# Performance work log

Measured on AMD Instinct MI355X. Metric: run time of the kernel, lower is better.

The kernel has to match this reference:

```python
import jax, jax.numpy as jnp
import numpy as np

NUM_DIRECTIONS = 100  # matches init_kwargs
N_POINTS = 200000


def setup_inputs() -> dict:
    key = jax.random.key(0)
    k1, k2 = jax.random.split(key)
    X = jax.random.normal(k1, (N_POINTS, 2), dtype=jnp.float32)
    Y = jax.random.normal(k2, (N_POINTS, 2), dtype=jnp.float32)
    return {"X": X, "Y": Y}


def _lines():
    # thetas = linspace(-pi/2, pi/2, K+1)[:-1]; lines[i] = (cos t_i, sin t_i)
    thetas = jnp.linspace(-np.pi / 2, np.pi / 2, NUM_DIRECTIONS + 1)[:-1]
    L = jnp.stack([jnp.cos(thetas), jnp.sin(thetas)], axis=1).astype(jnp.float32)  # [K, 2]
    return L


def reference(X, Y):
    # X, Y: [N, 2], [M, 2] persistence diagrams (birth, death)
    L = _lines()                                   # [K, 2]
    inv_norm = 1.0 / jnp.sum(L * L, axis=1)        # [K] (== 1 analytically, kept for fidelity)
    diag = jnp.array([0.5, 0.5], dtype=jnp.float32)

    # diagonal projections of each diagram: sum(point) * [0.5, 0.5]
    X_diag = jnp.sum(X, axis=1, keepdims=True) * diag  # [N, 2]
    Y_diag = jnp.sum(Y, axis=1, keepdims=True) * diag  # [M, 2]

    # batched line projections: replaces per-point dot-product loops
    proj_X = (X @ L.T) * inv_norm                  # [N, K]
    proj_Y = (Y @ L.T) * inv_norm                  # [M, K]
    proj_Xd = (X_diag @ L.T) * inv_norm            # [N, K]
    proj_Yd = (Y_diag @ L.T) * inv_norm            # [M, K]

    # 1D EMD per direction: sort both multisets, sum |diff|
    A = jnp.sort(jnp.concatenate([proj_X, proj_Yd], axis=0), axis=0)  # [N+M, K]
    B = jnp.sort(jnp.concatenate([proj_Y, proj_Xd], axis=0), axis=0)  # [N+M, K]

    total_cost = jnp.sum(jnp.abs(A - B)) / NUM_DIRECTIONS
    return total_cost
```

## Files before the change

kernel.cpp:

```cpp
#include <hip/hip_runtime.h>

#define KDIR 100
#define TILE 4096
#define NPASS 3
#define MBLK 256
#define MOUT 4096
#define MPT2 (MOUT / MBLK)

__device__ __forceinline__ unsigned encodeF(float f) {
  unsigned u = __float_as_uint(f);
  return u ^ ((u >> 31) ? 0xFFFFFFFFu : 0x80000000u);
}
__device__ __forceinline__ float decodeU(unsigned u) {
  return __uint_as_float(u ^ ((u >> 31) ? 0x80000000u : 0xFFFFFFFFu));
}

__global__ void k_table(float* tbl, double* part, int nSlots) {
  int k = threadIdx.x;
  const double PI = 3.14159265358979323846;
  if (k < KDIR) {
    double th = -PI * 0.5 + (double)k * (PI / (double)KDIR);
    float c = (float)cos(th), s = (float)sin(th);
    float invn = 1.0f / (c * c + s * s);
    tbl[k] = c; tbl[128 + k] = s; tbl[256 + k] = (c + s) * invn; tbl[384 + k] = invn;
  }
  if (k == 100) { tbl[100] = 0.5f; tbl[228] = 0.5f; tbl[484] = 1.0f; }
  for (int i = k; i < nSlots; i += 256) part[i] = 0.0;
}

__global__ __launch_bounds__(256) void k_build(const float* __restrict__ P, int n, int kIdx,
                                               const float* __restrict__ tbl,
                                               unsigned* __restrict__ dst,
                                               unsigned* __restrict__ counts, int T, int seg0) {
  __shared__ unsigned h[256];
  int tid = threadIdx.x;
  h[tid] = 0;
  __syncthreads();
  int dir = blockIdx.y;
  int k = kIdx + dir;
  float ck = tbl[k], sk = tbl[128 + k], inv = tbl[384 + k];
  int tile = blockIdx.x;
  int start = tile * TILE;
  int nItems = min(TILE, n - start);
  unsigned* d0 = dst + (size_t)dir * n + start;
  const float* p0 = P + 2 * (size_t)start;
  if (nItems == TILE) {
    const float4* p4 = (const float4*)p0;
    uint2* o2 = (uint2*)d0;
#pragma unroll
    for (int i = 0; i < 8; ++i) {
      float4 v = p4[i * 256 + tid];
      unsigned ua = encodeF((v.x * ck + v.y * sk) * inv);
      unsigned ub = encodeF((v.z * ck + v.w * sk) * inv);
      o2[i * 256 + tid] = make_uint2(ua, ub);
      atomicAdd(&h[(ua >> 8) & 255u], 1u);
      atomicAdd(&h[(ub >> 8) & 255u], 1u);
    }
  } else {
    for (int j = tid; j < nItems; j += 256) {
      float x = p0[2 * j], y = p0[2 * j + 1];
      unsigned u = encodeF((x * ck + y * sk) * inv);
      d0[j] = u;
      atomicAdd(&h[(u >> 8) & 255u], 1u);
    }
  }
  __syncthreads();
  counts[((size_t)(seg0 + dir) * 256 + tid) * T + tile] = h[tid];
}

__global__ __launch_bounds__(256) void k_hist8(const unsigned* __restrict__ keys,
                                               int L, int T, int shift,
                                               unsigned* __restrict__ counts) {
  __shared__ unsigned h[4][256];
  int tid = threadIdx.x;
  int w = tid >> 6;
  for (int i = tid; i < 4 * 256; i += 256) ((unsigned*)h)[i] = 0;
  __syncthreads();
  int seg = blockIdx.y, tile = blockIdx.x;
  const unsigned* base = keys + (size_t)seg * L + (size_t)tile * TILE;
  int nItems = min(TILE, L - tile * TILE);
  if (nItems == TILE) {
    const uint4* b4 = (const uint4*)base;
#pragma unroll
    for (int i = 0; i < 4; ++i) {
      uint4 v = b4[i * 256 + tid];
      atomicAdd(&h[w][(v.x >> shift) & 255u], 1u);
      atomicAdd(&h[w][(v.y >> shift) & 255u], 1u);
      atomicAdd(&h[w][(v.z >> shift) & 255u], 1u);
      atomicAdd(&h[w][(v.w >> shift) & 255u], 1u);
    }
  } else {
    for (int i = tid; i < nItems; i += 256)
      atomicAdd(&h[w][(base[i] >> shift) & 255u], 1u);
  }
  __syncthreads();
  counts[((size_t)seg * 256 + tid) * T + tile] =
      h[0][tid] + h[1][tid] + h[2][tid] + h[3][tid];
}

__global__ __launch_bounds__(256) void k_scanSeg(unsigned* __restrict__ counts, int T) {
  __shared__ unsigned tot[256];
  unsigned* c = counts + (size_t)blockIdx.x * 256 * T;
  int tid = threadIdx.x;
  int base = tid * T;
  unsigned sum = 0;
  for (int i = 0; i < T; ++i) sum += c[base + i];
  tot[tid] = sum;
  __syncthreads();
  for (int ofs = 1; ofs < 256; ofs <<= 1) {
    unsigned t = (tid >= ofs) ? tot[tid - ofs] : 0u;
    __syncthreads();
    tot[tid] += t;
    __syncthreads();
  }
  unsigned run = tot[tid] - sum;
  for (int i = 0; i < T; ++i) {
    unsigned v = c[base + i];
    c[base + i] = run;
    run += v;
  }
}

__global__ __launch_bounds__(256) void k_scatter8(const unsigned* __restrict__ src,
                                                  unsigned* __restrict__ dst,
                                                  int L, int T, int shift,
                                                  const unsigned* __restrict__ counts) {
  __shared__ unsigned runG[4][4][256];
  __shared__ unsigned diffD[256];
  __shared__ unsigned wsum[4];
  int tid = threadIdx.x;
  int lane = tid & 63, w = tid >> 6;
  int seg = blockIdx.y, tile = blockIdx.x;
  const unsigned* sbase = src + (size_t)seg * L + (size_t)tile * TILE;
  int nItems = min(TILE, L - tile * TILE);
  for (int i = tid; i < 4 * 4 * 256; i += 256) ((unsigned*)runG)[i] = 0;
  __syncthreads();
  unsigned kk[16];
  unsigned rr[16];
  unsigned long long laneLT = (1ull << lane) - 1ull;
  int jbase = w * (TILE / 4);
#pragma unroll
  for (int i = 0; i < 16; ++i) {
    int j = jbase + i * 64 + lane;
    kk[i] = (j < nItems) ? sbase[j] : 0xFFFFFFFFu;
  }
#pragma unroll
  for (int s = 0; s < 4; ++s) {
    unsigned long long mask[4];
    unsigned prev[4];
#pragma unroll
    for (int g = 0; g < 4; ++g) {
      int i = g * 4 + s;
      int j = jbase + i * 64 + lane;
      bool valid = j < nItems;
      unsigned long long act = __ballot(valid);
      unsigned d = (kk[i] >> shift) & 255u;
      unsigned long long m = act;
#pragma unroll
      for (int b = 0; b < 8; ++b) {
        unsigned long long bal = __ballot((d >> b) & 1);
        m &= ((d >> b) & 1) ? bal : ~bal;
      }
      mask[g] = m;
      prev[g] = runG[w][g][d];
    }
#pragma unroll
    for (int g = 0; g < 4; ++g) {
      int i = g * 4 + s;
      int j = jbase + i * 64 + lane;
      if (j < nItems) {
        unsigned d = (kk[i] >> shift) & 255u;
        unsigned r = (unsigned)__popcll(mask[g] & laneLT);
        rr[i] = prev[g] + r;
        if (r == 0) runG[w][g][d] = prev[g] + (unsigned)__popcll(mask[g]);
      }
    }
  }
  __syncthreads();
  {
    unsigned v[16];
#pragma unroll
    for (int w2 = 0; w2 < 4; ++w2)
#pragma unroll
      for (int g2 = 0; g2 < 4; ++g2) v[w2 * 4 + g2] = runG[w2][g2][tid];
    unsigned tot = 0;
#pragma unroll
    for (int i = 0; i < 16; ++i) {
      unsigned t = v[i];
      v[i] = tot;
      tot += t;
    }
    unsigned x = tot;
#pragma unroll
    for (int ofs = 1; ofs < 64; ofs <<= 1) {
      unsigned t = __shfl_up(x, ofs, 64);
      if (lane >= ofs) x += t;
    }
    if (lane == 63) wsum[w] = x;
    __syncthreads();
    unsigned basew = 0;
#pragma unroll
    for (int w2 = 0; w2 < 4; ++w2) basew += (w2 < w) ? wsum[w2] : 0u;
    unsigned localStart = basew + x - tot;
    diffD[tid] = counts[((size_t)seg * 256 + tid) * T + tile] - localStart;
#pragma unroll
    for (int w2 = 0; w2 < 4; ++w2)
#pragma unroll
      for (int g2 = 0; g2 < 4; ++g2)
        runG[w2][g2][tid] = v[w2 * 4 + g2] + localStart;
  }
  __syncthreads();
  unsigned lp[16];
#pragma unroll
  for (int i = 0; i < 16; ++i) {
    unsigned d = (kk[i] >> shift) & 255u;
    lp[i] = runG[w][i >> 2][d] + rr[i];
  }
  __syncthreads();
  unsigned* kbuf = &runG[0][0][0];
#pragma unroll
  for (int i = 0; i < 16; ++i) {
    int j = jbase + i * 64 + lane;
    if (j < nItems) kbuf[lp[i]] = kk[i];
  }
  __syncthreads();
  unsigned* dbase = dst + (size_t)seg * L;
#pragma unroll
  for (int i = 0; i < 16; ++i) {
    int pos = i * 256 + tid;
    if (pos < nItems) {
      unsigned k = kbuf[pos];
      unsigned d = (k >> shift) & 255u;
      dbase[diffD[d] + (unsigned)pos] = k;
    }
  }
}

__device__ __forceinline__ float scaledAt(const unsigned* __restrict__ s, int len, int j,
                                          float c, int rev) {
  return c * decodeU(s[rev ? (len - 1 - j) : j]);
}

__device__ int mergeSplit(const unsigned* __restrict__ U, int n,
                          const unsigned* __restrict__ sV, int m,
                          float c, int rev, int o) {
  int lo = o - m; if (lo < 0) lo = 0;
  int hi = o < n ? o : n;
  while (lo < hi) {
    int mid = (lo + hi + 1) >> 1;
    if (decodeU(U[mid - 1]) <= scaledAt(sV, m, o - mid, c, rev)) lo = mid;
    else hi = mid - 1;
  }
  return lo;
}

__global__ void k_splits(const unsigned* __restrict__ pX, const unsigned* __restrict__ pY,
                         const unsigned* __restrict__ sx, const unsigned* __restrict__ sy,
                         int N, int M, int k0, int mB,
                         const float* __restrict__ tbl, int* __restrict__ splits) {
  int b = blockIdx.x * blockDim.x + threadIdx.x;
  if (b >= mB) return;
  int kl = blockIdx.y;
  int kc = gridDim.y;
  float c = tbl[256 + k0 + kl];
  int rev = c < 0.0f ? 1 : 0;
  int Stot = N + M;
  int o = b * MOUT; if (o > Stot) o = Stot;
  const unsigned* U1 = pX + (size_t)kl * N;
  const unsigned* U2 = pY + (size_t)kl * M;
  splits[(size_t)kl * mB + b] = mergeSplit(U1, N, sy, M, c, rev, o);
  splits[((size_t)kc + kl) * mB + b] = mergeSplit(U2, M, sx, N, c, rev, o);
}

__device__ __forceinline__ int ldsSplit(const float* __restrict__ sArr, int aCnt, int bCnt,
                                        int o) {
  int lo = o - bCnt; if (lo < 0) lo = 0;
  int hi = o < aCnt ? o : aCnt;
  while (lo < hi) {
    int mid = (lo + hi + 1) >> 1;
    if (sArr[mid - 1] <= sArr[aCnt + o - mid]) lo = mid;
    else hi = mid - 1;
  }
  return lo;
}

__device__ __forceinline__ void merge8(const float* __restrict__ sArr, int aCnt, int bCnt,
                                       int la, int lb, float* m) {
  const float FMAX = 3.402823466e38f;
  float a[8], b[8];
#pragma unroll
  for (int j = 0; j < 8; ++j) {
    a[j] = (la + j < aCnt) ? sArr[la + j] : FMAX;
    b[j] = (lb + j < bCnt) ? sArr[aCnt + lb + j] : FMAX;
  }
#pragma unroll
  for (int j = 0; j < 8; ++j) m[j] = fminf(a[j], b[7 - j]);
#pragma unroll
  for (int d = 4; d > 0; d >>= 1) {
#pragma unroll
    for (int i = 0; i < 8; ++i) {
      if ((i & d) == 0 && (i | d) < 8) {
        float lo = fminf(m[i], m[i | d]);
        float hi = fmaxf(m[i], m[i | d]);
        m[i] = lo; m[i | d] = hi;
      }
    }
  }
}

__global__ __launch_bounds__(MBLK) void k_merge(const unsigned* __restrict__ pX,
                                                const unsigned* __restrict__ pY,
                                                const unsigned* __restrict__ sx,
                                                const unsigned* __restrict__ sy,
                                                int N, int M, int k0,
                                                const float* __restrict__ tbl,
                                                const int* __restrict__ splits, int mB,
                                                double* __restrict__ part) {
  __shared__ float sA[MOUT];
  __shared__ float sB[MOUT];
  __shared__ float red[MBLK];
  int kl = blockIdx.y;
  int kc = gridDim.y;
  float c = tbl[256 + k0 + kl];
  int rev = c < 0.0f ? 1 : 0;
  int Stot = N + M;
  int o0 = blockIdx.x * MOUT;
  int outCnt = min(MOUT, Stot - o0);
  const unsigned* U1 = pX + (size_t)kl * N;
  const unsigned* U2 = pY + (size_t)kl * M;
  int tid = threadIdx.x;
  int aLo = splits[(size_t)kl * mB + blockIdx.x];
  int aHi = splits[(size_t)kl * mB + blockIdx.x + 1];
  int a2Lo = splits[((size_t)kc + kl) * mB + blockIdx.x];
  int a2Hi = splits[((size_t)kc + kl) * mB + blockIdx.x + 1];
  int aCnt = aHi - aLo;
  int bLo = o0 - aLo, bCnt = outCnt - aCnt;
  int a2Cnt = a2Hi - a2Lo;
  int b2Lo = o0 - a2Lo, b2Cnt = outCnt - a2Cnt;
  for (int i = tid; i < aCnt; i += MBLK) sA[i] = decodeU(U1[aLo + i]);
  for (int i = tid; i < bCnt; i += MBLK) {
    int j = bLo + i;
    sA[aCnt + i] = c * decodeU(sy[rev ? (M - 1 - j) : j]);
  }
  for (int i = tid; i < a2Cnt; i += MBLK) sB[i] = decodeU(U2[a2Lo + i]);
  for (int i = tid; i < b2Cnt; i += MBLK) {
    int j = b2Lo + i;
    sB[a2Cnt + i] = c * decodeU(sx[rev ? (N - 1 - j) : j]);
  }
  __syncthreads();
  float acc = 0.0f;
#pragma unroll
  for (int half = 0; half < 2; ++half) {
    int lo0 = tid * MPT2 + half * 8;
    if (lo0 < outCnt) {
      int cnt = min(8, outCnt - lo0);
      int la = ldsSplit(sA, aCnt, bCnt, lo0);
      int lb = lo0 - la;
      int la2 = ldsSplit(sB, a2Cnt, b2Cnt, lo0);
      int lb2 = lo0 - la2;
      float mA[8], mB2[8];
      merge8(sA, aCnt, bCnt, la, lb, mA);
      merge8(sB, a2Cnt, b2Cnt, la2, lb2, mB2);
#pragma unroll
      for (int j = 0; j < 8; ++j)
        if (j < cnt) acc += fabsf(mA[j] - mB2[j]);
    }
  }
  red[tid] = acc;
  __syncthreads();
  for (int ofs = MBLK / 2; ofs > 0; ofs >>= 1) {
    if (tid < ofs) red[tid] += red[tid + ofs];
    __syncthreads();
  }
  if (tid == 0) {
    size_t slot = (size_t)(k0 + kl) * gridDim.x + blockIdx.x;
    part[slot] += (double)red[0];
  }
}

__global__ __launch_bounds__(256) void k_final(const double* __restrict__ part, int nSlots,
                                               float* __restrict__ out) {
  __shared__ double red[256];
  int tid = threadIdx.x;
  double s = 0.0;
  for (int i = tid; i < nSlots; i += 256) s += part[i];
  red[tid] = s;
  __syncthreads();
  for (int ofs = 128; ofs > 0; ofs >>= 1) {
    if (tid < ofs) red[tid] += red[tid + ofs];
    __syncthreads();
  }
  if (tid == 0) out[0] = (float)(red[0] / (double)KDIR);
}

extern "C" void kernel_launch(void* const* d_in, const int* in_sizes, int n_in,
                              void* d_out, int out_size, void* d_ws, size_t ws_size,
                              hipStream_t stream) {
  const float* X = (const float*)d_in[0];
  const float* Y = (const float*)d_in[1];
  int N = in_sizes[0] / 2;
  int M = in_sizes[1] / 2;

  char* ws = (char*)d_ws;
  size_t off = 0;
  auto alloc = [&](size_t b) -> void* {
    void* p = ws + off;
    off += (b + 255) & ~(size_t)255;
    return p;
  };
  float* tbl = (float*)alloc(512 * sizeof(float));
  unsigned* sPing = (unsigned*)alloc((size_t)(N + M) * 4);
  unsigned* sPong = (unsigned*)alloc((size_t)(N + M) * 4);

  int Tn = (N + TILE - 1) / TILE;
  int Tm = (M + TILE - 1) / TILE;
  int Tmax = Tn > Tm ? Tn : Tm;
  int mx = N > M ? N : M;
  int mBlocksAll = (N + M + MOUT - 1) / MOUT;
  int mB = mBlocksAll + 1;
  int nSlots = KDIR * mBlocksAll;
  int* splits = (int*)alloc((size_t)2 * KDIR * mB * 4);
  double* part = (double*)alloc((size_t)nSlots * 8);

  size_t perDir = (size_t)(N + M) * 8 + (size_t)2 * 256 * Tmax * 4;
  size_t reserve = (size_t)2 * mx * 8 + (size_t)2 * 256 * Tmax * 4;
  size_t remain = ws_size > off ? ws_size - off : 0;
  remain = remain > reserve ? remain - reserve : 0;
  int Kc = (int)(remain / perDir);
  if (Kc > KDIR) Kc = KDIR;
  if (Kc < 1) Kc = 1;
  int maxSegs = 2 * Kc + 2;
  unsigned* counts8 = (unsigned*)alloc((size_t)maxSegs * 256 * Tmax * 4);
  unsigned* cPing = (unsigned*)alloc(((size_t)Kc * (N + M) + 2 * (size_t)mx) * 4);
  unsigned* cPong = (unsigned*)alloc(((size_t)Kc * (N + M) + 2 * (size_t)mx) * 4);

  k_table<<<1, 256, 0, stream>>>(tbl, part, nSlots);

  auto sortJob = [&](unsigned* ping, unsigned* pong, int segs, int L) {
    int T = (L + TILE - 1) / TILE;
    unsigned* s = pong;
    unsigned* d = ping;
    for (int p = 0; p < NPASS; ++p) {
      int shift = 8 * (p + 1);
      if (p > 0)
        k_hist8<<<dim3(T, segs), 256, 0, stream>>>(s, L, T, shift, counts8);
      k_scanSeg<<<segs, 256, 0, stream>>>(counts8, T);
      k_scatter8<<<dim3(T, segs), 256, 0, stream>>>(s, d, L, T, shift, counts8);
      unsigned* t = s; s = d; d = t;
    }
  };

  bool fused = (N == M) && (Kc == KDIR);

  if (fused) {
    unsigned* dXin = cPong + (size_t)2 * KDIR * N;
    unsigned* dYin = dXin + N;
    k_build<<<dim3(Tn, KDIR), 256, 0, stream>>>(X, N, 0, tbl, cPong, counts8, Tn, 0);
    k_build<<<dim3(Tn, KDIR), 256, 0, stream>>>(Y, N, 0, tbl, cPong + (size_t)KDIR * N,
                                                counts8, Tn, KDIR);
    k_build<<<dim3(Tn, 1), 256, 0, stream>>>(X, N, 100, tbl, dXin, counts8, Tn, 2 * KDIR);
    k_build<<<dim3(Tn, 1), 256, 0, stream>>>(Y, N, 100, tbl, dYin, counts8, Tn, 2 * KDIR + 1);
    sortJob(cPing, cPong, 2 * KDIR + 2, N);
    unsigned* pX = cPing;
    unsigned* pY = cPing + (size_t)KDIR * N;
    unsigned* dX = cPing + (size_t)2 * KDIR * N;
    unsigned* dY = dX + N;
    k_splits<<<dim3((mB + 255) / 256, KDIR), 256, 0, stream>>>(pX, pY, dX, dY, N, M, 0, mB,
                                                               tbl, splits);
    k_merge<<<dim3(mBlocksAll, KDIR), MBLK, 0, stream>>>(pX, pY, dX, dY, N, M, 0, tbl,
                                                         splits, mB, part);
  } else {
    if (N == M) {
      k_build<<<dim3(Tn, 1), 256, 0, stream>>>(X, N, 100, tbl, sPong, counts8, Tn, 0);
      k_build<<<dim3(Tn, 1), 256, 0, stream>>>(Y, N, 100, tbl, sPong + N, counts8, Tn, 1);
      sortJob(sPing, sPong, 2, N);
    } else {
      k_build<<<dim3(Tn, 1), 256, 0, stream>>>(X, N, 100, tbl, sPong, counts8, Tn, 0);
      sortJob(sPing, sPong, 1, N);
      k_build<<<dim3(Tm, 1), 256, 0, stream>>>(Y, M, 100, tbl, sPong + N, counts8, Tm, 0);
      sortJob(sPing + N, sPong + N, 1, M);
    }
    for (int k0 = 0; k0 < KDIR; k0 += Kc) {
      int kc = (KDIR - k0 < Kc) ? (KDIR - k0) : Kc;
      unsigned* pXin = cPong;
      unsigned* pYin = cPong + (size_t)kc * N;
      unsigned* pX = cPing;
      unsigned* pY = cPing + (size_t)kc * N;
      if (N == M) {
        k_build<<<dim3(Tn, kc), 256, 0, stream>>>(X, N, k0, tbl, pXin, counts8, Tn, 0);
        k_build<<<dim3(Tn, kc), 256, 0, stream>>>(Y, N, k0, tbl, pYin, counts8, Tn, kc);
        sortJob(cPing, cPong, 2 * kc, N);
      } else {
        k_build<<<dim3(Tn, kc), 256, 0, stream>>>(X, N, k0, tbl, pXin, counts8, Tn, 0);
        sortJob(pX, pXin, kc, N);
        k_build<<<dim3(Tm, kc), 256, 0, stream>>>(Y, M, k0, tbl, pYin, counts8, Tm, 0);
        sortJob(pY, pYin, kc, M);
      }
      k_splits<<<dim3((mB + 255) / 256, kc), 256, 0, stream>>>(pX, pY, sPing, sPing + N,
                                                               N, M, k0, mB, tbl, splits);
      k_merge<<<dim3(mBlocksAll, kc), MBLK, 0, stream>>>(pX, pY, sPing, sPing + N, N, M, k0,
                                                         tbl, splits, mB, part);
    }
  }
  k_final<<<1, 256, 0, stream>>>(part, nSlots, (float*)d_out);
}
```

Before: 988.1 us.

## Fuse next-pass histogram into radix scatter and widen merge blocks

The radix scatter kernel now also builds the histogram for the next digit. It counts runs of equal (tile, digit) pairs with wave ballots and adds them to a second counts buffer with atomics. This removes the separate histogram pass over the keys for passes 2 and 3 in the fused path, at the cost of two memsets, a doubled counts buffer and global atomics. The merge kernel also moves to 512 threads with 8 outputs per thread, replacing 256 threads that each did two 8-element chunks.

```diff
diff --git a/kernel.cpp b/kernel.cpp
--- a/kernel.cpp
+++ b/kernel.cpp
@@ -3,9 +3,9 @@
 #define KDIR 100
 #define TILE 4096
 #define NPASS 3
-#define MBLK 256
+#define MBLK 512
 #define MOUT 4096
-#define MPT2 (MOUT / MBLK)
+#define MPT 8
 
 __device__ __forceinline__ unsigned encodeF(float f) {
   unsigned u = __float_as_uint(f);
@@ -124,7 +124,9 @@
 __global__ __launch_bounds__(256) void k_scatter8(const unsigned* __restrict__ src,
                                                   unsigned* __restrict__ dst,
                                                   int L, int T, int shift,
-                                                  const unsigned* __restrict__ counts) {
+                                                  const unsigned* __restrict__ counts,
+                                                  unsigned* __restrict__ nextCounts,
+                                                  int shift2) {
   __shared__ unsigned runG[4][4][256];
   __shared__ unsigned diffD[256];
   __shared__ unsigned wsum[4];
@@ -228,10 +230,28 @@
 #pragma unroll
   for (int i = 0; i < 16; ++i) {
     int pos = i * 256 + tid;
-    if (pos < nItems) {
-      unsigned k = kbuf[pos];
+    bool valid = pos < nItems;
+    unsigned k = 0, g = 0, d2 = 0;
+    if (valid) {
+      k = kbuf[pos];
       unsigned d = (k >> shift) & 255u;
-      dbase[diffD[d] + (unsigned)pos] = k;
+      g = diffD[d] + (unsigned)pos;
+      dbase[g] = k;
+      d2 = (k >> shift2) & 255u;
+    }
+    if (nextCounts) {
+      unsigned pid = ((g >> 12) << 8) | d2;
+      unsigned prevPid = __shfl_up(pid, 1, 64);
+      bool leader = valid && (lane == 0 || pid != prevPid);
+      unsigned long long lm = __ballot(leader);
+      unsigned long long vm = __ballot(valid);
+      unsigned long long bounds = lm | ~vm;
+      unsigned long long above = bounds & ~((2ull << lane) - 1ull);
+      if (leader) {
+        int nxt = above ? __builtin_ctzll(above) : 64;
+        unsigned cnt = (unsigned)(nxt - lane);
+        atomicAdd(&nextCounts[((size_t)seg * 256 + d2) * T + (g >> 12)], cnt);
+      }
     }
   }
 }
@@ -349,22 +369,19 @@
   }
   __syncthreads();
   float acc = 0.0f;
-#pragma unroll
-  for (int half = 0; half < 2; ++half) {
-    int lo0 = tid * MPT2 + half * 8;
-    if (lo0 < outCnt) {
-      int cnt = min(8, outCnt - lo0);
-      int la = ldsSplit(sA, aCnt, bCnt, lo0);
-      int lb = lo0 - la;
-      int la2 = ldsSplit(sB, a2Cnt, b2Cnt, lo0);
-      int lb2 = lo0 - la2;
-      float mA[8], mB2[8];
-      merge8(sA, aCnt, bCnt, la, lb, mA);
-      merge8(sB, a2Cnt, b2Cnt, la2, lb2, mB2);
-#pragma unroll
-      for (int j = 0; j < 8; ++j)
-        if (j < cnt) acc += fabsf(mA[j] - mB2[j]);
-    }
+  int lo0 = tid * MPT;
+  if (lo0 < outCnt) {
+    int cnt = min(MPT, outCnt - lo0);
+    int la = ldsSplit(sA, aCnt, bCnt, lo0);
+    int lb = lo0 - la;
+    int la2 = ldsSplit(sB, a2Cnt, b2Cnt, lo0);
+    int lb2 = lo0 - la2;
+    float mA[8], mB2[8];
+    merge8(sA, aCnt, bCnt, la, lb, mA);
+    merge8(sB, a2Cnt, b2Cnt, la2, lb2, mB2);
+#pragma unroll
+    for (int j = 0; j < 8; ++j)
+      if (j < cnt) acc += fabsf(mA[j] - mB2[j]);
   }
   red[tid] = acc;
   __syncthreads();
@@ -422,15 +439,17 @@
   int* splits = (int*)alloc((size_t)2 * KDIR * mB * 4);
   double* part = (double*)alloc((size_t)nSlots * 8);
 
-  size_t perDir = (size_t)(N + M) * 8 + (size_t)2 * 256 * Tmax * 4;
-  size_t reserve = (size_t)2 * mx * 8 + (size_t)2 * 256 * Tmax * 4;
+  size_t perDir = (size_t)(N + M) * 8 + (size_t)4 * 256 * Tmax * 4;
+  size_t reserve = (size_t)2 * mx * 8 + (size_t)4 * 256 * Tmax * 4;
   size_t remain = ws_size > off ? ws_size - off : 0;
   remain = remain > reserve ? remain - reserve : 0;
   int Kc = (int)(remain / perDir);
   if (Kc > KDIR) Kc = KDIR;
   if (Kc < 1) Kc = 1;
   int maxSegs = 2 * Kc + 2;
-  unsigned* counts8 = (unsigned*)alloc((size_t)maxSegs * 256 * Tmax * 4);
+  size_t cntElems = (size_t)maxSegs * 256 * Tmax;
+  unsigned* countsA = (unsigned*)alloc(cntElems * 4);
+  unsigned* countsB = (unsigned*)alloc(cntElems * 4);
   unsigned* cPing = (unsigned*)alloc(((size_t)Kc * (N + M) + 2 * (size_t)mx) * 4);
   unsigned* cPong = (unsigned*)alloc(((size_t)Kc * (N + M) + 2 * (size_t)mx) * 4);
 
@@ -443,9 +462,10 @@
     for (int p = 0; p < NPASS; ++p) {
       int shift = 8 * (p + 1);
       if (p > 0)
-        k_hist8<<<dim3(T, segs), 256, 0, stream>>>(s, L, T, shift, counts8);
-      k_scanSeg<<<segs, 256, 0, stream>>>(counts8, T);
-      k_scatter8<<<dim3(T, segs), 256, 0, stream>>>(s, d, L, T, shift, counts8);
+        k_hist8<<<dim3(T, segs), 256, 0, stream>>>(s, L, T, shift, countsA);
+      k_scanSeg<<<segs, 256, 0, stream>>>(countsA, T);
+      k_scatter8<<<dim3(T, segs), 256, 0, stream>>>(s, d, L, T, shift, countsA,
+                                                    (unsigned*)nullptr, 0);
       unsigned* t = s; s = d; d = t;
     }
   };
@@ -455,12 +475,25 @@
   if (fused) {
     unsigned* dXin = cPong + (size_t)2 * KDIR * N;
     unsigned* dYin = dXin + N;
-    k_build<<<dim3(Tn, KDIR), 256, 0, stream>>>(X, N, 0, tbl, cPong, counts8, Tn, 0);
+    k_build<<<dim3(Tn, KDIR), 256, 0, stream>>>(X, N, 0, tbl, cPong, countsA, Tn, 0);
     k_build<<<dim3(Tn, KDIR), 256, 0, stream>>>(Y, N, 0, tbl, cPong + (size_t)KDIR * N,
-                                                counts8, Tn, KDIR);
-    k_build<<<dim3(Tn, 1), 256, 0, stream>>>(X, N, 100, tbl, dXin, counts8, Tn, 2 * KDIR);
-    k_build<<<dim3(Tn, 1), 256, 0, stream>>>(Y, N, 100, tbl, dYin, counts8, Tn, 2 * KDIR + 1);
-    sortJob(cPing, cPong, 2 * KDIR + 2, N);
+                                                countsA, Tn, KDIR);
+    k_build<<<dim3(Tn, 1), 256, 0, stream>>>(X, N, 100, tbl, dXin, countsA, Tn, 2 * KDIR);
+    k_build<<<dim3(Tn, 1), 256, 0, stream>>>(Y, N, 100, tbl, dYin, countsA, Tn, 2 * KDIR + 1);
+    int segs = 2 * KDIR + 2;
+    int T = Tn;
+    size_t cntBytes = (size_t)segs * 256 * T * 4;
+    hipMemsetAsync(countsB, 0, cntBytes, stream);
+    k_scanSeg<<<segs, 256, 0, stream>>>(countsA, T);
+    k_scatter8<<<dim3(T, segs), 256, 0, stream>>>(cPong, cPing, N, T, 8, countsA,
+                                                  countsB, 16);
+    k_scanSeg<<<segs, 256, 0, stream>>>(countsB, T);
+    hipMemsetAsync(countsA, 0, cntBytes, stream);
+    k_scatter8<<<dim3(T, segs), 256, 0, stream>>>(cPing, cPong, N, T, 16, countsB,
+                                                  countsA, 24);
+    k_scanSeg<<<segs, 256, 0, stream>>>(countsA, T);
+    k_scatter8<<<dim3(T, segs), 256, 0, stream>>>(cPong, cPing, N, T, 24, countsA,
+                                                  (unsigned*)nullptr, 0);
     unsigned* pX = cPing;
     unsigned* pY = cPing + (size_t)KDIR * N;
     unsigned* dX = cPing + (size_t)2 * KDIR * N;
@@ -471,13 +504,13 @@
                                                          splits, mB, part);
   } else {
     if (N == M) {
-      k_build<<<dim3(Tn, 1), 256, 0, stream>>>(X, N, 100, tbl, sPong, counts8, Tn, 0);
-      k_build<<<dim3(Tn, 1), 256, 0, stream>>>(Y, N, 100, tbl, sPong + N, counts8, Tn, 1);
+      k_build<<<dim3(Tn, 1), 256, 0, stream>>>(X, N, 100, tbl, sPong, countsA, Tn, 0);
+      k_build<<<dim3(Tn, 1), 256, 0, stream>>>(Y, N, 100, tbl, sPong + N, countsA, Tn, 1);
       sortJob(sPing, sPong, 2, N);
     } else {
-      k_build<<<dim3(Tn, 1), 256, 0, stream>>>(X, N, 100, tbl, sPong, counts8, Tn, 0);
+      k_build<<<dim3(Tn, 1), 256, 0, stream>>>(X, N, 100, tbl, sPong, countsA, Tn, 0);
       sortJob(sPing, sPong, 1, N);
-      k_build<<<dim3(Tm, 1), 256, 0, stream>>>(Y, M, 100, tbl, sPong + N, counts8, Tm, 0);
+      k_build<<<dim3(Tm, 1), 256, 0, stream>>>(Y, M, 100, tbl, sPong + N, countsA, Tm, 0);
       sortJob(sPing + N, sPong + N, 1, M);
     }
     for (int k0 = 0; k0 < KDIR; k0 += Kc) {
@@ -487,13 +520,13 @@
       unsigned* pX = cPing;
       unsigned* pY = cPing + (size_t)kc * N;
       if (N == M) {
-        k_build<<<dim3(Tn, kc), 256, 0, stream>>>(X, N, k0, tbl, pXin, counts8, Tn, 0);
-        k_build<<<dim3(Tn, kc), 256, 0, stream>>>(Y, N, k0, tbl, pYin, counts8, Tn, kc);
+        k_build<<<dim3(Tn, kc), 256, 0, stream>>>(X, N, k0, tbl, pXin, countsA, Tn, 0);
+        k_build<<<dim3(Tn, kc), 256, 0, stream>>>(Y, N, k0, tbl, pYin, countsA, Tn, kc);
         sortJob(cPing, cPong, 2 * kc, N);
       } else {
-        k_build<<<dim3(Tn, kc), 256, 0, stream>>>(X, N, k0, tbl, pXin, counts8, Tn, 0);
+        k_build<<<dim3(Tn, kc), 256, 0, stream>>>(X, N, k0, tbl, pXin, countsA, Tn, 0);
         sortJob(pX, pXin, kc, N);
-        k_build<<<dim3(Tm, kc), 256, 0, stream>>>(Y, M, k0, tbl, pYin, counts8, Tm, 0);
+        k_build<<<dim3(Tm, kc), 256, 0, stream>>>(Y, M, k0, tbl, pYin, countsA, Tm, 0);
         sortJob(pY, pYin, kc, M);
       }
       k_splits<<<dim3((mB + 255) / 256, kc), 256, 0, stream>>>(pX, pY, sPing, sPing + N,
```

New measurement: 950.7 us. 3.8% less time.
